# Kernel optimization log

Measured on AMD Instinct MI355X. Metric: run time of the kernel, lower is better.

## Reference

```python
import jax, jax.numpy as jnp
import numpy as np


def setup_inputs() -> dict:
    key = jax.random.key(0)
    k1, k2, k3 = jax.random.split(key, 3)
    B, S, D_IN, D_OUT = 8, 512, 4096, 16384
    x = jax.random.normal(k1, (B, S, D_IN), dtype=jnp.float32)
    # int8 weights stored as int32 values in [-128, 127] (int8 semantics)
    weight_int8 = jax.random.randint(k2, (D_OUT, D_IN), -128, 128, dtype=jnp.int32)
    # per-tensor scale, e.g. max_abs/127 of an fp32 weight with std ~0.02
    weight_scale = jnp.float32(0.02 * 4.0 / 127.0)
    bias = jax.random.normal(k3, (D_OUT,), dtype=jnp.float32) * 0.01
    return {"x": x, "weight_int8": weight_int8, "weight_scale": weight_scale, "bias": bias}


def reference(x, weight_int8, weight_scale, bias):
    # dequantize: materialize fp32 weight (per-tensor scale, zero_point = 0)
    weight_fp32 = weight_int8.astype(jnp.float32) * weight_scale  # [O, I]
    # F.linear: y = x @ W^T + b
    out = jnp.einsum("bsi,oi->bso", x, weight_fp32) + bias
    return out
```

## Files before the change

kernel.cpp:

```cpp
#include <hip/hip_runtime.h>
#include <stdint.h>
#include <stddef.h>

typedef __attribute__((ext_vector_type(4)))  int   i32x4;
typedef __attribute__((ext_vector_type(8)))  short bf16x8;
typedef __attribute__((ext_vector_type(4)))  float f32x4;
typedef __attribute__((ext_vector_type(4)))  float f32x4v;
typedef __attribute__((ext_vector_type(4)))  unsigned short u16x4;

__device__ __forceinline__ unsigned short f2bf(float f) {
    union { float f; unsigned u; } v; v.f = f;
    unsigned r = v.u + 0x7FFFu + ((v.u >> 16) & 1u);
    return (unsigned short)(r >> 16);
}

__device__ __forceinline__ void gload_lds16(const void* g, void* l) {
    __builtin_amdgcn_global_load_lds(
        (const __attribute__((address_space(1))) void*)(g),
        (__attribute__((address_space(3))) void*)(l), 16, 0, 0);
}

__device__ __forceinline__ int pack4(float a, float b, float c, float d, float inv) {
    int r0 = ((int)rintf(a * inv)) & 255;
    int r1 = ((int)rintf(b * inv)) & 255;
    int r2 = ((int)rintf(c * inv)) & 255;
    int r3 = ((int)rintf(d * inv)) & 255;
    return r0 | (r1 << 8) | (r2 << 16) | (r3 << 24);
}

__global__ void cvt_x_q8(const float* __restrict__ x, signed char* __restrict__ xq,
                         float* __restrict__ sx, int K) {
    const int row = blockIdx.x;
    const int t   = threadIdx.x;
    const float* xr = x + (size_t)row * K;
    const int ng = K / 1024;

    f32x4v v[8];
    float am = 0.f;
#pragma unroll
    for (int i = 0; i < 8; ++i) {
        if (i < ng) {
            v[i] = __builtin_nontemporal_load(&((const f32x4v*)xr)[i * 256 + t]);
            am = fmaxf(am, fmaxf(fmaxf(fabsf(v[i][0]), fabsf(v[i][1])),
                                 fmaxf(fabsf(v[i][2]), fabsf(v[i][3]))));
        }
    }
#pragma unroll
    for (int m = 32; m >= 1; m >>= 1) am = fmaxf(am, __shfl_xor(am, m, 64));
    __shared__ float red[4];
    const int w = t >> 6;
    if ((t & 63) == 0) red[w] = am;
    __syncthreads();
    am = fmaxf(fmaxf(red[0], red[1]), fmaxf(red[2], red[3]));

    const float inv = (am > 0.f) ? 127.0f / am : 0.f;
    if (t == 0) sx[row] = (am > 0.f) ? am / 127.0f : 0.f;

    int* oq = (int*)(xq + (size_t)row * K);
#pragma unroll
    for (int i = 0; i < 8; ++i)
        if (i < ng) oq[i * 256 + t] = pack4(v[i][0], v[i][1], v[i][2], v[i][3], inv);
}

__global__ void cvt_w_q8(const int* __restrict__ w, signed char* __restrict__ o, int n4) {
    int i = blockIdx.x * blockDim.x + threadIdx.x;
    int stride = gridDim.x * blockDim.x;
    for (; i < n4; i += stride) {
        i32x4 a = __builtin_nontemporal_load(&((const i32x4*)w)[i]);
        ((int*)o)[i] = (a[0] & 255) | ((a[1] & 255) << 8) | ((a[2] & 255) << 16) | ((a[3] & 255) << 24);
    }
}

#define BM8 256
#define BN8 256
#define BKQ 128

__global__ __launch_bounds__(512, 2) void gemm8p_i8(
    const signed char* __restrict__ A,
    const signed char* __restrict__ Bw,
    const float* __restrict__ sx,
    const float* __restrict__ scale_p,
    const float* __restrict__ bias,
    float* __restrict__ C,
    int M, int N, int K)
{
    __shared__ __align__(16) char smem[131072];

    const int t    = threadIdx.x;
    const int lane = t & 63;
    const int w    = t >> 6;
    const int wm   = w >> 2;
    const int wn   = w & 3;

    const int ntn = N / BN8;
    const int ntm = M / BM8;
    int nwg = gridDim.x, bid = blockIdx.x;
    int tm, tn;
    if (((nwg & 7) == 0) && (ntm % 8 == 0)) {
        const int x = bid & 7, c = bid >> 3;
        const int tmB = ntm >> 3;
        tm = x * tmB + (c % tmB);
        tn = c / tmB;
    } else if ((nwg & 7) == 0) {
        int swz = (bid & 7) * (nwg >> 3) + (bid >> 3);
        tm = swz / ntn; tn = swz % ntn;
    } else {
        tm = bid / ntn; tn = bid % ntn;
    }
    const int row0 = tm * BM8;
    const int col0 = tn * BN8;

    const int Kb = K;
    const int NT = K / BKQ;

    const int srow = w * 8 + (lane >> 3);
    const int sc2  = ((lane & 7) ^ (lane >> 3)) * 16;
    const int ldsLaneOff = w * 1024 + lane * 16;

    const char* aG = (const char*)A + (size_t)(row0 + srow) * Kb + sc2;
    const char* bG = (const char*)Bw + (size_t)(col0 + srow) * Kb + sc2;

    const int q    = lane >> 4;
    const int lr   = lane & 15;
    const int swzr = (lr & 7) << 4;

    i32x4 acc[8][4] = {};
    i32x4 aF[4][2], aS[4][2], bF[2][2], bS[2][2];

#define STG(gbase, h, tj, buf, region) do {                                   \
    const char* _g = (gbase) + (size_t)(h) * 128 * Kb + (size_t)(tj) * 128;   \
    char* _l = &smem[(buf) * 65536 + (region) * 16384 + ldsLaneOff];          \
    gload_lds16(_g, _l);                                                      \
    gload_lds16(_g + (size_t)64 * Kb, _l + 8192);                             \
} while (0)

#define RDA(buf, mi, ks) \
    (*(const i32x4*)&smem[(buf) * 65536 + wm * 16384 + ((mi) * 16 + lr) * 128 \
                          + ((((ks) << 6) | (q << 4)) ^ swzr)])
#define RDB(buf, nj, ks) \
    (*(const i32x4*)&smem[(buf) * 65536 + (2 + (wn >> 1)) * 16384              \
                          + ((wn & 1) * 64 + (nj) * 16 + lr) * 128             \
                          + ((((ks) << 6) | (q << 4)) ^ swzr)])

#define MFMA_(a, b, c) (c) = __builtin_amdgcn_mfma_i32_16x16x64_i8((a), (b), (c), 0, 0, 0)
#define BAR() __builtin_amdgcn_s_barrier()
#define FENCE() asm volatile("" ::: "memory")
#define VM4() asm volatile("s_waitcnt vmcnt(4)" ::: "memory")
#define VM0() asm volatile("s_waitcnt vmcnt(0)" ::: "memory")
#define VMNONE() do { } while (0)

#define TILE_STEP(tt, bb, stB, stA2, VMW) do {                                        \
                              \
    _Pragma("unroll") for (int mi = 0; mi < 4; ++mi) {                                \
        aF[mi][0] = RDA(bb, mi, 0); aF[mi][1] = RDA(bb, mi, 1); }                     \
    _Pragma("unroll") for (int nj = 0; nj < 2; ++nj) {                                \
        bF[nj][0] = RDB(bb, nj, 0); bF[nj][1] = RDB(bb, nj, 1); }                     \
    if (stB) STG(bG, 0, (tt) + 1, (bb) ^ 1, 2);                                       \
    __builtin_amdgcn_s_setprio(1);                                                    \
    _Pragma("unroll") for (int mi = 0; mi < 4; ++mi)                                  \
    _Pragma("unroll") for (int nj = 0; nj < 2; ++nj) {                                \
        MFMA_(aF[mi][0], bF[nj][0], acc[mi][nj]);                                     \
        MFMA_(aF[mi][1], bF[nj][1], acc[mi][nj]); }                                   \
    __builtin_amdgcn_s_setprio(0);                                                    \
                                 \
    _Pragma("unroll") for (int nj = 0; nj < 2; ++nj) {                                \
        bS[nj][0] = RDB(bb, 2 + nj, 0); bS[nj][1] = RDB(bb, 2 + nj, 1); }             \
    if (stB) STG(bG, 1, (tt) + 1, (bb) ^ 1, 3);                                       \
    __builtin_amdgcn_s_setprio(1);                                                    \
    _Pragma("unroll") for (int mi = 0; mi < 4; ++mi)                                  \
    _Pragma("unroll") for (int nj = 0; nj < 2; ++nj) {                                \
        MFMA_(aF[mi][0], bS[nj][0], acc[mi][2 + nj]);                                 \
        MFMA_(aF[mi][1], bS[nj][1], acc[mi][2 + nj]); }                               \
    __builtin_amdgcn_s_setprio(0);                                                    \
                                                \
    _Pragma("unroll") for (int mi = 0; mi < 4; ++mi) {                                \
        aS[mi][0] = RDA(bb, 4 + mi, 0); aS[mi][1] = RDA(bb, 4 + mi, 1); }             \
    __builtin_amdgcn_s_setprio(1);                                                    \
    _Pragma("unroll") for (int mi = 0; mi < 4; ++mi)                                  \
    _Pragma("unroll") for (int nj = 0; nj < 2; ++nj) {                                \
        MFMA_(aS[mi][0], bS[nj][0], acc[4 + mi][2 + nj]);                             \
        MFMA_(aS[mi][1], bS[nj][1], acc[4 + mi][2 + nj]); }                           \
    __builtin_amdgcn_s_setprio(0);                                                    \
    BAR(); FENCE();              \
                    \
    _Pragma("unroll") for (int nj = 0; nj < 2; ++nj) {                                \
        bF[nj][0] = RDB(bb, nj, 0); bF[nj][1] = RDB(bb, nj, 1); }                     \
    if (stA2) { STG(aG, 0, (tt) + 2, (bb), 0); STG(aG, 1, (tt) + 2, (bb), 1); }       \
    __builtin_amdgcn_s_setprio(1);                                                    \
    _Pragma("unroll") for (int mi = 0; mi < 4; ++mi)                                  \
    _Pragma("unroll") for (int nj = 0; nj < 2; ++nj) {                                \
        MFMA_(aS[mi][0], bF[nj][0], acc[4 + mi][nj]);                                 \
        MFMA_(aS[mi][1], bF[nj][1], acc[4 + mi][nj]); }                               \
    __builtin_amdgcn_s_setprio(0);                                                    \
    VMW();                                                                            \
    BAR(); FENCE();              \
} while (0)

    STG(aG, 0, 0, 0, 0); STG(aG, 1, 0, 0, 1);
    STG(bG, 0, 0, 0, 2); STG(bG, 1, 0, 0, 3);
    STG(aG, 0, 1, 1, 0); STG(aG, 1, 1, 1, 1);
    VM4();
    BAR(); FENCE();

    for (int tt = 0; tt < NT - 2; tt += 2) {
        TILE_STEP(tt,     0, 1, 1, VM4);
        TILE_STEP(tt + 1, 1, 1, 1, VM4);
    }
    TILE_STEP(NT - 2, 0, 1, 0, VM0);
    TILE_STEP(NT - 1, 1, 0, 0, VMNONE);

    const float s = scale_p[0];
    float bv[4];
#pragma unroll
    for (int nj = 0; nj < 4; ++nj) bv[nj] = bias[col0 + wn * 64 + nj * 16 + lr];
#pragma unroll
    for (int mi = 0; mi < 8; ++mi) {
        const int rbase = row0 + wm * 128 + mi * 16 + q * 4;
        float sxr[4];
#pragma unroll
        for (int j = 0; j < 4; ++j) sxr[j] = sx[rbase + j] * s;
#pragma unroll
        for (int nj = 0; nj < 4; ++nj) {
            const int col = col0 + wn * 64 + nj * 16 + lr;
#pragma unroll
            for (int j = 0; j < 4; ++j)
                C[(size_t)(rbase + j) * N + col] = (float)acc[mi][nj][j] * sxr[j] + bv[nj];
        }
    }
#undef STG
#undef RDA
#undef RDB
#undef TILE_STEP
}

#define BM 128
#define BN 128
#define BK 64

__global__ __launch_bounds__(256, 2) void gemm_fused(
    const float* __restrict__ A,
    const int* __restrict__ Bw,
    const float* __restrict__ scale_p,
    const float* __restrict__ bias,
    float* __restrict__ C,
    int M, int N, int K)
{
    __shared__ unsigned short As[BM * BK];
    __shared__ unsigned short Bs[BN * BK];
    const int t = threadIdx.x, lane = t & 63, w = t >> 6;
    const int wm = w >> 1, wn = w & 1;
    int nwg = gridDim.x, bid = blockIdx.x;
    int swz = (nwg % 8 == 0) ? ((bid & 7) * (nwg >> 3) + (bid >> 3)) : bid;
    const int ntn = N / BN;
    const int row0 = (swz / ntn) * BM, col0 = (swz % ntn) * BN;
    f32x4 acc[4][4] = {};
    const int lr = lane & 15, lkbase = (lane >> 4) * 8;

    for (int kt = 0; kt < K; kt += BK) {
#pragma unroll
        for (int i = 0; i < 8; ++i) {
            const int r = i * 16 + (t >> 4), c = (t & 15) * 4;
            f32x4v v = *(const f32x4v*)&A[(size_t)(row0 + r) * K + kt + c];
            u16x4 o; o[0] = f2bf(v[0]); o[1] = f2bf(v[1]); o[2] = f2bf(v[2]); o[3] = f2bf(v[3]);
            *(u16x4*)&As[r * BK + c] = o;
        }
#pragma unroll
        for (int i = 0; i < 8; ++i) {
            const int r = i * 16 + (t >> 4), c = (t & 15) * 4;
            i32x4 v = *(const i32x4*)&Bw[(size_t)(col0 + r) * K + kt + c];
            u16x4 o; o[0] = f2bf((float)v[0]); o[1] = f2bf((float)v[1]);
                     o[2] = f2bf((float)v[2]); o[3] = f2bf((float)v[3]);
            *(u16x4*)&Bs[r * BK + c] = o;
        }
        __syncthreads();
#pragma unroll
        for (int ks = 0; ks < 2; ++ks) {
            bf16x8 af[4], bfr[4];
#pragma unroll
            for (int m = 0; m < 4; ++m) af[m] = *(const bf16x8*)&As[(wm * 64 + m * 16 + lr) * BK + lkbase + ks * 32];
#pragma unroll
            for (int n = 0; n < 4; ++n) bfr[n] = *(const bf16x8*)&Bs[(wn * 64 + n * 16 + lr) * BK + lkbase + ks * 32];
#pragma unroll
            for (int m = 0; m < 4; ++m)
#pragma unroll
                for (int n = 0; n < 4; ++n)
                    acc[m][n] = __builtin_amdgcn_mfma_f32_16x16x32_bf16(af[m], bfr[n], acc[m][n], 0, 0, 0);
        }
        __syncthreads();
    }
    const float s = scale_p[0];
    const int lq4 = (lane >> 4) * 4;
#pragma unroll
    for (int m = 0; m < 4; ++m)
#pragma unroll
        for (int n = 0; n < 4; ++n) {
            const int col = col0 + wn * 64 + n * 16 + lr;
            const float bv = bias[col];
#pragma unroll
            for (int j = 0; j < 4; ++j) {
                const int row = row0 + wm * 64 + m * 16 + lq4 + j;
                C[(size_t)row * N + col] = acc[m][n][j] * s + bv;
            }
        }
}

extern "C" void kernel_launch(void* const* d_in, const int* in_sizes, int n_in,
                              void* d_out, int out_size, void* d_ws, size_t ws_size,
                              hipStream_t stream) {
    const float* x     = (const float*)d_in[0];
    const int*   w8    = (const int*)d_in[1];
    const float* scale = (const float*)d_in[2];
    const float* bias  = (const float*)d_in[3];
    float* out = (float*)d_out;

    const int N = in_sizes[3];
    const int K = (int)((long)in_sizes[1] / N);
    const int M = (int)((long)in_sizes[0] / K);

    const size_t needA = (size_t)M * K;
    const size_t needB = (size_t)N * K;
    const size_t needS = (size_t)M * sizeof(float);
    const int NT = K / BKQ;

    const bool okShape = (M % BM8 == 0) && (N % BN8 == 0) && (K % BKQ == 0) &&
                         (K % 1024 == 0) && (K / 1024 <= 8) &&
                         (NT >= 4) && ((NT & 1) == 0);

    if (okShape && ws_size >= needA + needB + needS) {
        signed char* Aq = (signed char*)d_ws;
        signed char* Bq = Aq + needA;
        float*       sx = (float*)(Bq + needB);
        cvt_x_q8<<<M, 256, 0, stream>>>(x, Aq, sx, K);
        cvt_w_q8<<<4096, 256, 0, stream>>>(w8, Bq, (int)((size_t)N * K / 4));
        const int nblocks = (M / BM8) * (N / BN8);
        gemm8p_i8<<<nblocks, 512, 0, stream>>>(Aq, Bq, sx, scale, bias, out, M, N, K);
    } else {
        const int nblocks = (M / BM) * (N / BN);
        gemm_fused<<<nblocks, 256, 0, stream>>>(x, w8, scale, bias, out, M, N, K);
    }
}
```

Before: 316.9 us.

## Shrink int8 GEMM block tile to 128x128 with higher occupancy target

Replaces the 256x256 int8 MFMA GEMM tile with a 128x128 tile. Each of the 8 waves now computes a 64x32 sub-tile, the LDS footprint is halved to 64KB, and launch bounds request 4 blocks per CU. The staging pipeline is simplified to one A and one B load group per K-step, with waitcnt adjusted to match. The goal is more blocks in flight and better latency hiding, at the cost of half the data reuse per tile, more L2/global traffic, and possible register pressure or spills under the tighter launch bound.

```diff
diff --git a/kernel.cpp b/kernel.cpp
--- a/kernel.cpp
+++ b/kernel.cpp
@@ -71,11 +71,11 @@
     }
 }
 
-#define BM8 256
-#define BN8 256
+#define BMT 128
+#define BNT 128
 #define BKQ 128
 
-__global__ __launch_bounds__(512, 2) void gemm8p_i8(
+__global__ __launch_bounds__(512, 4) void gemm128_i8(
     const signed char* __restrict__ A,
     const signed char* __restrict__ Bw,
     const float* __restrict__ sx,
@@ -84,7 +84,7 @@
     float* __restrict__ C,
     int M, int N, int K)
 {
-    __shared__ __align__(16) char smem[131072];
+    __shared__ __align__(16) char smem[65536];
 
     const int t    = threadIdx.x;
     const int lane = t & 63;
@@ -92,8 +92,8 @@
     const int wm   = w >> 2;
     const int wn   = w & 3;
 
-    const int ntn = N / BN8;
-    const int ntm = M / BM8;
+    const int ntn = N / BNT;
+    const int ntm = M / BMT;
     int nwg = gridDim.x, bid = blockIdx.x;
     int tm, tn;
     if (((nwg & 7) == 0) && (ntm % 8 == 0)) {
@@ -107,8 +107,8 @@
     } else {
         tm = bid / ntn; tn = bid % ntn;
     }
-    const int row0 = tm * BM8;
-    const int col0 = tn * BN8;
+    const int row0 = tm * BMT;
+    const int col0 = tn * BNT;
 
     const int Kb = K;
     const int NT = K / BKQ;
@@ -124,110 +124,85 @@
     const int lr   = lane & 15;
     const int swzr = (lr & 7) << 4;
 
-    i32x4 acc[8][4] = {};
-    i32x4 aF[4][2], aS[4][2], bF[2][2], bS[2][2];
-
-#define STG(gbase, h, tj, buf, region) do {                                   \
-    const char* _g = (gbase) + (size_t)(h) * 128 * Kb + (size_t)(tj) * 128;   \
-    char* _l = &smem[(buf) * 65536 + (region) * 16384 + ldsLaneOff];          \
+    i32x4 acc[4][2] = {};
+    i32x4 aF[4][2], bB[2][2];
+
+#define STG128(gbase, tj, buf, regoff) do {                                   \
+    const char* _g = (gbase) + (size_t)(tj) * 128;                            \
+    char* _l = &smem[(buf) * 32768 + (regoff) + ldsLaneOff];                  \
     gload_lds16(_g, _l);                                                      \
     gload_lds16(_g + (size_t)64 * Kb, _l + 8192);                             \
 } while (0)
 
 #define RDA(buf, mi, ks) \
-    (*(const i32x4*)&smem[(buf) * 65536 + wm * 16384 + ((mi) * 16 + lr) * 128 \
+    (*(const i32x4*)&smem[(buf) * 32768 + ((wm * 64 + (mi) * 16 + lr) * 128) \
                           + ((((ks) << 6) | (q << 4)) ^ swzr)])
 #define RDB(buf, nj, ks) \
-    (*(const i32x4*)&smem[(buf) * 65536 + (2 + (wn >> 1)) * 16384              \
-                          + ((wn & 1) * 64 + (nj) * 16 + lr) * 128             \
+    (*(const i32x4*)&smem[(buf) * 32768 + 16384                               \
+                          + ((wn * 32 + (nj) * 16 + lr) * 128)                \
                           + ((((ks) << 6) | (q << 4)) ^ swzr)])
 
 #define MFMA_(a, b, c) (c) = __builtin_amdgcn_mfma_i32_16x16x64_i8((a), (b), (c), 0, 0, 0)
 #define BAR() __builtin_amdgcn_s_barrier()
 #define FENCE() asm volatile("" ::: "memory")
-#define VM4() asm volatile("s_waitcnt vmcnt(4)" ::: "memory")
+#define VM2() asm volatile("s_waitcnt vmcnt(2)" ::: "memory")
 #define VM0() asm volatile("s_waitcnt vmcnt(0)" ::: "memory")
 #define VMNONE() do { } while (0)
 
 #define TILE_STEP(tt, bb, stB, stA2, VMW) do {                                        \
-                              \
+    if (stB) STG128(bG, (tt) + 1, (bb) ^ 1, 16384);                                   \
     _Pragma("unroll") for (int mi = 0; mi < 4; ++mi) {                                \
         aF[mi][0] = RDA(bb, mi, 0); aF[mi][1] = RDA(bb, mi, 1); }                     \
     _Pragma("unroll") for (int nj = 0; nj < 2; ++nj) {                                \
-        bF[nj][0] = RDB(bb, nj, 0); bF[nj][1] = RDB(bb, nj, 1); }                     \
-    if (stB) STG(bG, 0, (tt) + 1, (bb) ^ 1, 2);                                       \
+        bB[nj][0] = RDB(bb, nj, 0); bB[nj][1] = RDB(bb, nj, 1); }                     \
     __builtin_amdgcn_s_setprio(1);                                                    \
+    _Pragma("unroll") for (int ks = 0; ks < 2; ++ks)                                  \
     _Pragma("unroll") for (int mi = 0; mi < 4; ++mi)                                  \
-    _Pragma("unroll") for (int nj = 0; nj < 2; ++nj) {                                \
-        MFMA_(aF[mi][0], bF[nj][0], acc[mi][nj]);                                     \
-        MFMA_(aF[mi][1], bF[nj][1], acc[mi][nj]); }                                   \
+        MFMA_(aF[mi][ks], bB[0][ks], acc[mi][0]);                                     \
     __builtin_amdgcn_s_setprio(0);                                                    \
-                                 \
-    _Pragma("unroll") for (int nj = 0; nj < 2; ++nj) {                                \
-        bS[nj][0] = RDB(bb, 2 + nj, 0); bS[nj][1] = RDB(bb, 2 + nj, 1); }             \
-    if (stB) STG(bG, 1, (tt) + 1, (bb) ^ 1, 3);                                       \
+    BAR(); FENCE();                    \
+    if (stA2) STG128(aG, (tt) + 2, (bb), 0);                                          \
     __builtin_amdgcn_s_setprio(1);                                                    \
+    _Pragma("unroll") for (int ks = 0; ks < 2; ++ks)                                  \
     _Pragma("unroll") for (int mi = 0; mi < 4; ++mi)                                  \
-    _Pragma("unroll") for (int nj = 0; nj < 2; ++nj) {                                \
-        MFMA_(aF[mi][0], bS[nj][0], acc[mi][2 + nj]);                                 \
-        MFMA_(aF[mi][1], bS[nj][1], acc[mi][2 + nj]); }                               \
-    __builtin_amdgcn_s_setprio(0);                                                    \
-                                                \
-    _Pragma("unroll") for (int mi = 0; mi < 4; ++mi) {                                \
-        aS[mi][0] = RDA(bb, 4 + mi, 0); aS[mi][1] = RDA(bb, 4 + mi, 1); }             \
-    __builtin_amdgcn_s_setprio(1);                                                    \
-    _Pragma("unroll") for (int mi = 0; mi < 4; ++mi)                                  \
-    _Pragma("unroll") for (int nj = 0; nj < 2; ++nj) {                                \
-        MFMA_(aS[mi][0], bS[nj][0], acc[4 + mi][2 + nj]);                             \
-        MFMA_(aS[mi][1], bS[nj][1], acc[4 + mi][2 + nj]); }                           \
-    __builtin_amdgcn_s_setprio(0);                                                    \
-    BAR(); FENCE();              \
-                    \
-    _Pragma("unroll") for (int nj = 0; nj < 2; ++nj) {                                \
-        bF[nj][0] = RDB(bb, nj, 0); bF[nj][1] = RDB(bb, nj, 1); }                     \
-    if (stA2) { STG(aG, 0, (tt) + 2, (bb), 0); STG(aG, 1, (tt) + 2, (bb), 1); }       \
-    __builtin_amdgcn_s_setprio(1);                                                    \
-    _Pragma("unroll") for (int mi = 0; mi < 4; ++mi)                                  \
-    _Pragma("unroll") for (int nj = 0; nj < 2; ++nj) {                                \
-        MFMA_(aS[mi][0], bF[nj][0], acc[4 + mi][nj]);                                 \
-        MFMA_(aS[mi][1], bF[nj][1], acc[4 + mi][nj]); }                               \
+        MFMA_(aF[mi][ks], bB[1][ks], acc[mi][1]);                                     \
     __builtin_amdgcn_s_setprio(0);                                                    \
     VMW();                                                                            \
     BAR(); FENCE();              \
 } while (0)
 
-    STG(aG, 0, 0, 0, 0); STG(aG, 1, 0, 0, 1);
-    STG(bG, 0, 0, 0, 2); STG(bG, 1, 0, 0, 3);
-    STG(aG, 0, 1, 1, 0); STG(aG, 1, 1, 1, 1);
-    VM4();
+    STG128(aG, 0, 0, 0);
+    STG128(bG, 0, 0, 16384);
+    STG128(aG, 1, 1, 0);
+    VM2();
     BAR(); FENCE();
 
     for (int tt = 0; tt < NT - 2; tt += 2) {
-        TILE_STEP(tt,     0, 1, 1, VM4);
-        TILE_STEP(tt + 1, 1, 1, 1, VM4);
+        TILE_STEP(tt,     0, 1, 1, VM2);
+        TILE_STEP(tt + 1, 1, 1, 1, VM2);
     }
     TILE_STEP(NT - 2, 0, 1, 0, VM0);
     TILE_STEP(NT - 1, 1, 0, 0, VMNONE);
 
     const float s = scale_p[0];
-    float bv[4];
-#pragma unroll
-    for (int nj = 0; nj < 4; ++nj) bv[nj] = bias[col0 + wn * 64 + nj * 16 + lr];
-#pragma unroll
-    for (int mi = 0; mi < 8; ++mi) {
-        const int rbase = row0 + wm * 128 + mi * 16 + q * 4;
+    float bv[2];
+#pragma unroll
+    for (int nj = 0; nj < 2; ++nj) bv[nj] = bias[col0 + wn * 32 + nj * 16 + lr];
+#pragma unroll
+    for (int mi = 0; mi < 4; ++mi) {
+        const int rbase = row0 + wm * 64 + mi * 16 + q * 4;
         float sxr[4];
 #pragma unroll
         for (int j = 0; j < 4; ++j) sxr[j] = sx[rbase + j] * s;
 #pragma unroll
-        for (int nj = 0; nj < 4; ++nj) {
-            const int col = col0 + wn * 64 + nj * 16 + lr;
+        for (int nj = 0; nj < 2; ++nj) {
+            const int col = col0 + wn * 32 + nj * 16 + lr;
 #pragma unroll
             for (int j = 0; j < 4; ++j)
                 C[(size_t)(rbase + j) * N + col] = (float)acc[mi][nj][j] * sxr[j] + bv[nj];
         }
     }
-#undef STG
+#undef STG128
 #undef RDA
 #undef RDB
 #undef TILE_STEP
@@ -322,7 +297,7 @@
     const size_t needS = (size_t)M * sizeof(float);
     const int NT = K / BKQ;
 
-    const bool okShape = (M % BM8 == 0) && (N % BN8 == 0) && (K % BKQ == 0) &&
+    const bool okShape = (M % BMT == 0) && (N % BNT == 0) && (K % BKQ == 0) &&
                          (K % 1024 == 0) && (K / 1024 <= 8) &&
                          (NT >= 4) && ((NT & 1) == 0);
 
@@ -332,8 +307,8 @@
         float*       sx = (float*)(Bq + needB);
         cvt_x_q8<<<M, 256, 0, stream>>>(x, Aq, sx, K);
         cvt_w_q8<<<4096, 256, 0, stream>>>(w8, Bq, (int)((size_t)N * K / 4));
-        const int nblocks = (M / BM8) * (N / BN8);
-        gemm8p_i8<<<nblocks, 512, 0, stream>>>(Aq, Bq, sx, scale, bias, out, M, N, K);
+        const int nblocks = (M / BMT) * (N / BNT);
+        gemm128_i8<<<nblocks, 512, 0, stream>>>(Aq, Bq, sx, scale, bias, out, M, N, K);
     } else {
         const int nblocks = (M / BM) * (N / BN);
         gemm_fused<<<nblocks, 256, 0, stream>>>(x, w8, scale, bias, out, M, N, K);
```

New measurement: 339.4 us. 7.1% more time.
